# Performance work log

Measured on AMD Instinct MI355X. Metric: run time of the kernel, lower is better.

The kernel has to match this reference:

```python
import jax, jax.numpy as jnp
import numpy as np
from jax.scipy.linalg import solve_triangular

NUM_EMBEDDINGS = 512
EMBEDDING_DIM = 64
SPARSITY = 5
COMMITMENT_COST = 0.25


def batch_omp(data, dictionary, max_nonzero):
    """Batch OMP. data: (M, B), dictionary: (M, N). Returns coeffs (N, B)."""
    M, B = data.shape
    Dt = dictionary.T                       # (N, M)
    G = Dt @ dictionary                     # (N, N) Gram matrix
    h_bar = (Dt @ data).T                   # (B, N)
    h = h_bar
    x = jnp.zeros_like(h_bar)               # (B, N)
    L = jnp.ones((B, 1, 1), data.dtype)     # growing Cholesky factor
    mask = jnp.zeros(h_bar.shape, dtype=bool)
    I = None                                # selected atom indices (B, k)
    bidx = jnp.arange(B)
    for k in range(1, max_nonzero + 1):     # small fixed unroll (5 iters)
        index = jnp.argmax(jnp.abs(h * (~mask)), axis=1)   # (B,)
        mask = mask.at[bidx, index].set(True)
        if k > 1:
            # G[I_b, index_b] for each batch element -> (B, k-1, 1)
            G_stack = G[I, index[:, None]][..., None]
            w = solve_triangular(L, G_stack, lower=True)   # (B, k-1, 1)
            wT = jnp.swapaxes(w, 1, 2)                     # (B, 1, k-1)
            w_corner = jnp.sqrt(jnp.clip(1.0 - jnp.sum(wT ** 2, axis=2, keepdims=True), 0.0))
            top = jnp.concatenate([L, jnp.zeros((B, k - 1, 1), L.dtype)], axis=2)
            bot = jnp.concatenate([wT, w_corner], axis=2)
            L = jnp.concatenate([top, bot], axis=1)        # (B, k, k)
            I = jnp.concatenate([I, index[:, None]], axis=1)
        else:
            I = index[:, None]
        h_stack = jnp.take_along_axis(h_bar, I, axis=1)[..., None]  # (B, k, 1)
        y = solve_triangular(L, h_stack, lower=True)
        x_stack = solve_triangular(jnp.swapaxes(L, 1, 2), y, lower=False)  # (B, k, 1)
        x = x.at[bidx[:, None], I].set(x_stack[..., 0])
        beta = jnp.einsum('bk,bkn->bn', x_stack[..., 0], G[I])  # (B, N)
        h = h_bar - beta
    return x.T                              # (N, B)


def setup_inputs() -> dict:
    key = jax.random.key(0)
    k1, k2 = jax.random.split(key)
    z_e = jax.random.normal(k1, (32, EMBEDDING_DIM, 32, 32), dtype=jnp.float32)
    D = jax.random.normal(k2, (EMBEDDING_DIM, NUM_EMBEDDINGS), dtype=jnp.float32)
    D = D / jnp.linalg.norm(D, axis=0)      # column-normalized atoms (as _normalize_dictionary)
    return {"z_e": z_e, "dictionary": D}


def reference(z_e, dictionary):
    # permute BCHW -> BHWC, then flat view to (embedding_dim, -1) row-major (as torch .view)
    z_perm = jnp.transpose(z_e, (0, 2, 3, 1))          # (B, H, W, C)
    input_shape = z_perm.shape
    ze_flat = z_perm.reshape(EMBEDDING_DIM, -1)        # (M, Btokens)
    coefficients = batch_omp(ze_flat, dictionary, SPARSITY)  # (N, Btokens)
    z_dl = (dictionary @ coefficients).reshape(input_shape)
    e_latent_loss = jnp.mean((jax.lax.stop_gradient(z_dl) - z_perm) ** 2)
    dl_latent_loss = jnp.mean((z_dl - jax.lax.stop_gradient(z_perm)) ** 2)
    loss = COMMITMENT_COST * e_latent_loss + dl_latent_loss
    z_out = z_perm + jax.lax.stop_gradient(z_dl - z_perm)   # straight-through
    return (jnp.transpose(z_out, (0, 3, 1, 2)), loss, coefficients)
```

## Files before the change

### kernel.cpp

```cpp
#include <hip/hip_runtime.h>

#define B_TOTAL 32768
#define NATOM   512
#define MDIM    64
#define KS      5

__global__ void k_perm(const float* __restrict__ ze, float* __restrict__ dT) {
    const int n   = blockIdx.x >> 4;
    const int hw0 = (blockIdx.x & 15) * 64;
    const int t   = threadIdx.x;
    __shared__ float lds[64][65];
#pragma unroll
    for (int r = 0; r < 16; ++r) {
        int id = r * 256 + t;
        int c = id >> 6, i = id & 63;
        lds[c][i] = ze[n * 65536 + c * 1024 + hw0 + i];
    }
    __syncthreads();
#pragma unroll
    for (int r = 0; r < 16; ++r) {
        int id = r * 256 + t;
        int c = id & 63, j = id >> 6;
        int hw = hw0 + j;
        int h = hw >> 5, w = hw & 31;
        int m = (n << 1) | (h >> 4);
        int b = ((h & 15) << 11) | (w << 6) | c;
        dT[m * 32768 + b] = lds[c][j];
    }
}

__global__ void k_gram(const float* __restrict__ D, float* __restrict__ G,
                       float* __restrict__ acc) {
    const int i = blockIdx.x;
    const int t = threadIdx.x;
    __shared__ float col[MDIM];
    if (t < MDIM) col[t] = D[t * NATOM + i];
    __syncthreads();
    for (int j = t; j < NATOM; j += 256) {
        float s = 0.f;
#pragma unroll
        for (int m = 0; m < MDIM; ++m) s = fmaf(col[m], D[m * NATOM + j], s);
        G[i * NATOM + j] = s;
    }
    if (i == 0 && t == 0) *acc = 0.f;
}

__launch_bounds__(256, 2)
__global__ void k_omp(const float* __restrict__ data, const float* __restrict__ D,
                      const float* __restrict__ G, int* __restrict__ idx_out,
                      float* __restrict__ val_out) {
    const int t    = threadIdx.x;
    const int lane = t & 63;
    const int wv   = t >> 6;
    const int b0   = blockIdx.x * 32;

    __shared__ __align__(16) float data_s[32][68];
    __shared__ __align__(16) float stage[4][2048];
    __shared__ int   idx_s[KS][32];
    __shared__ float val_s[KS][32];

#pragma unroll
    for (int r = 0; r < 8; ++r) {
        int id = r * 256 + t;
        int m = id >> 5, bb = id & 31;
        data_s[bb][m] = data[m * B_TOTAL + b0 + bb];
    }
    __syncthreads();

    const float4* __restrict__ D4 = (const float4*)D;
    const float4* __restrict__ G4 = (const float4*)G;

    float4 acc[8][2];
#pragma unroll
    for (int bb = 0; bb < 8; ++bb) {
        acc[bb][0] = make_float4(0.f, 0.f, 0.f, 0.f);
        acc[bb][1] = make_float4(0.f, 0.f, 0.f, 0.f);
    }
    const int bwbase = wv * 8;

#pragma unroll 4
    for (int c = 0; c < 16; ++c) {
        float4 df[4][2];
#pragma unroll
        for (int mm = 0; mm < 4; ++mm) {
            df[mm][0] = D4[(c * 4 + mm) * 128 + lane];
            df[mm][1] = D4[(c * 4 + mm) * 128 + 64 + lane];
        }
#pragma unroll
        for (int bb = 0; bb < 8; ++bb) {
            const float4 dv = *(const float4*)&data_s[bwbase + bb][c * 4];
            const float dm[4] = {dv.x, dv.y, dv.z, dv.w};
#pragma unroll
            for (int mm = 0; mm < 4; ++mm) {
                acc[bb][0].x = fmaf(df[mm][0].x, dm[mm], acc[bb][0].x);
                acc[bb][0].y = fmaf(df[mm][0].y, dm[mm], acc[bb][0].y);
                acc[bb][0].z = fmaf(df[mm][0].z, dm[mm], acc[bb][0].z);
                acc[bb][0].w = fmaf(df[mm][0].w, dm[mm], acc[bb][0].w);
                acc[bb][1].x = fmaf(df[mm][1].x, dm[mm], acc[bb][1].x);
                acc[bb][1].y = fmaf(df[mm][1].y, dm[mm], acc[bb][1].y);
                acc[bb][1].z = fmaf(df[mm][1].z, dm[mm], acc[bb][1].z);
                acc[bb][1].w = fmaf(df[mm][1].w, dm[mm], acc[bb][1].w);
            }
        }
    }

    const int g = lane >> 3;
    const int p = lane & 7;
    float hb[64];
#pragma unroll
    for (int r = 0; r < 2; ++r) {
        __syncthreads();
#pragma unroll
        for (int q2 = 0; q2 < 4; ++q2) {
            int bb = r * 4 + q2;
            *(float4*)&stage[wv][q2 * 512 + 4 * lane]       = acc[bb][0];
            *(float4*)&stage[wv][q2 * 512 + 256 + 4 * lane] = acc[bb][1];
        }
        __syncthreads();
        if ((g >> 2) == r) {
#pragma unroll
            for (int q = 0; q < 16; ++q) {
                const float4 v =
                    *(const float4*)&stage[wv][(g & 3) * 512 + 32 * q + 4 * p];
                hb[4 * q + 0] = v.x;
                hb[4 * q + 1] = v.y;
                hb[4 * q + 2] = v.z;
                hb[4 * q + 3] = v.w;
            }
        }
    }

    float key[64];
#pragma unroll
    for (int e = 0; e < 64; ++e) key[e] = fabsf(hb[e]);

    unsigned msk0 = 0u, msk1 = 0u;
    int   I[KS];
    float xs[KS];
    float gsel[KS];
    float Lm[15];

#pragma unroll
    for (int k = 0; k < KS; ++k) {
        float bv = key[0]; int be = 0; float bhb = hb[0];
#pragma unroll
        for (int e = 1; e < 64; ++e) {
            bool gt = key[e] > bv;
            bv  = gt ? key[e] : bv;
            be  = gt ? e      : be;
            bhb = gt ? hb[e]  : bhb;
        }
        int bn = 32 * (be >> 2) + 4 * p + (be & 3);
#pragma unroll
        for (int off = 1; off < 8; off <<= 1) {
            float ov  = __shfl_xor(bv, off);
            int   on  = __shfl_xor(bn, off);
            float ohb = __shfl_xor(bhb, off);
            bool take = (ov > bv) || (ov == bv && on < bn);
            bv = take ? ov : bv; bn = take ? on : bn; bhb = take ? ohb : bhb;
        }
        const int nsel = bn;
        I[k]    = nsel;
        gsel[k] = bhb;

        {
            int own  = (nsel >> 2) & 7;
            int esel = ((nsel >> 5) << 2) | (nsel & 3);
            if (p == own) {
                if (esel < 32) msk0 |= 1u << esel;
                else           msk1 |= 1u << (esel - 32);
            }
        }

        if (k > 0) {
            float gk[KS - 1], w[KS - 1];
#pragma unroll
            for (int ti = 0; ti < KS - 1; ++ti)
                if (ti < k) gk[ti] = G[I[ti] * NATOM + nsel];
#pragma unroll
            for (int r = 0; r < KS - 1; ++r) {
                if (r < k) {
                    float s = gk[r];
#pragma unroll
                    for (int cc = 0; cc < KS - 1; ++cc)
                        if (cc < r) s -= Lm[r * (r + 1) / 2 + cc] * w[cc];
                    w[r] = s / Lm[r * (r + 1) / 2 + r];
                }
            }
            float s2 = 0.f;
#pragma unroll
            for (int r = 0; r < KS - 1; ++r) if (r < k) s2 += w[r] * w[r];
            float wc = sqrtf(fmaxf(0.f, 1.f - s2));
#pragma unroll
            for (int cc = 0; cc < KS - 1; ++cc)
                if (cc < k) Lm[k * (k + 1) / 2 + cc] = w[cc];
            Lm[k * (k + 1) / 2 + k] = wc;
        } else {
            Lm[0] = 1.f;
        }

        float y[KS];
#pragma unroll
        for (int r = 0; r <= k; ++r) {
            float s = gsel[r];
#pragma unroll
            for (int cc = 0; cc < r; ++cc) s -= Lm[r * (r + 1) / 2 + cc] * y[cc];
            y[r] = s / Lm[r * (r + 1) / 2 + r];
        }
#pragma unroll
        for (int r = k; r >= 0; --r) {
            float s = y[r];
#pragma unroll
            for (int cc = r + 1; cc <= k; ++cc) s -= Lm[cc * (cc + 1) / 2 + r] * xs[cc];
            xs[r] = s / Lm[r * (r + 1) / 2 + r];
        }

        if (k < KS - 1) {
#pragma unroll
            for (int q = 0; q < 16; ++q) {
                float bx = 0.f, by = 0.f, bz = 0.f, bw = 0.f;
#pragma unroll
                for (int ti = 0; ti < KS - 1; ++ti) {
                    if (ti <= k) {
                        const float4 gc = G4[I[ti] * 128 + 8 * q + p];
                        bx = fmaf(xs[ti], gc.x, bx);
                        by = fmaf(xs[ti], gc.y, by);
                        bz = fmaf(xs[ti], gc.z, bz);
                        bw = fmaf(xs[ti], gc.w, bw);
                    }
                }
                {
                    float d0 = hb[4 * q + 0] - bx;
                    float d1 = hb[4 * q + 1] - by;
                    float d2 = hb[4 * q + 2] - bz;
                    float d3 = hb[4 * q + 3] - bw;
                    const int e0 = 4 * q;
                    bool m0 = (e0 + 0 < 32) ? ((msk0 >> (e0 + 0)) & 1u) : ((msk1 >> (e0 - 32)) & 1u);
                    bool m1 = (e0 + 1 < 32) ? ((msk0 >> (e0 + 1)) & 1u) : ((msk1 >> (e0 + 1 - 32)) & 1u);
                    bool m2 = (e0 + 2 < 32) ? ((msk0 >> (e0 + 2)) & 1u) : ((msk1 >> (e0 + 2 - 32)) & 1u);
                    bool m3 = (e0 + 3 < 32) ? ((msk0 >> (e0 + 3)) & 1u) : ((msk1 >> (e0 + 3 - 32)) & 1u);
                    key[e0 + 0] = m0 ? -1.f : fabsf(d0);
                    key[e0 + 1] = m1 ? -1.f : fabsf(d1);
                    key[e0 + 2] = m2 ? -1.f : fabsf(d2);
                    key[e0 + 3] = m3 ? -1.f : fabsf(d3);
                }
            }
        }
    }

    if (p == 0) {
#pragma unroll
        for (int k = 0; k < KS; ++k) {
            idx_s[k][wv * 8 + g] = I[k];
            val_s[k][wv * 8 + g] = xs[k];
        }
    }
    __syncthreads();
    if (t < KS * 32) {
        int k = t >> 5, bb = t & 31;
        idx_out[k * B_TOTAL + b0 + bb] = idx_s[k][bb];
        val_out[k * B_TOTAL + b0 + bb] = val_s[k][bb];
    }
}

__global__ void k_coeff(const int* __restrict__ idx, const float* __restrict__ val,
                        float* __restrict__ coeff) {
    const int bblk = blockIdx.x >> 3;
    const int jc   = blockIdx.x & 7;
    const int b    = bblk * 256 + threadIdx.x;
    int   I[KS]; float V[KS];
#pragma unroll
    for (int k = 0; k < KS; ++k) {
        I[k] = idx[k * B_TOTAL + b];
        V[k] = val[k * B_TOTAL + b];
    }
    const int j0 = jc * 64;
#pragma unroll 4
    for (int j = j0; j < j0 + 64; ++j) {
        float w = 0.f;
#pragma unroll
        for (int k = 0; k < KS; ++k) w = (I[k] == j) ? V[k] : w;
        coeff[j * B_TOTAL + b] = w;
    }
}

__global__ void k_recon(const float* __restrict__ dataT, const float* __restrict__ D,
                        const int* __restrict__ idx, const float* __restrict__ val,
                        float* __restrict__ zout, float* __restrict__ acc) {
    const int n   = blockIdx.x >> 4;
    const int hw0 = (blockIdx.x & 15) * 64;
    const int t   = threadIdx.x;
    __shared__ float lds[64][65];
    float sq = 0.f;
#pragma unroll
    for (int r = 0; r < 16; ++r) {
        int id = r * 256 + t;
        int c = id & 63, j = id >> 6;
        int f = n * 65536 + (hw0 + j) * 64 + c;
        int b = f & 32767;
        int m = f >> 15;
        float zdl = 0.f;
#pragma unroll
        for (int k = 0; k < KS; ++k) {
            int   a = idx[k * B_TOTAL + b];
            float v = val[k * B_TOTAL + b];
            zdl = fmaf(v, D[m * NATOM + a], zdl);
        }
        float zp   = dataT[f];
        float diff = zdl - zp;
        lds[c][j] = zp + diff;
        sq = fmaf(diff, diff, sq);
    }
    __syncthreads();
#pragma unroll
    for (int r = 0; r < 16; ++r) {
        int id = r * 256 + t;
        int cc = id >> 6, i = id & 63;
        zout[n * 65536 + cc * 1024 + hw0 + i] = lds[cc][i];
    }
#pragma unroll
    for (int off = 32; off > 0; off >>= 1) sq += __shfl_xor(sq, off);
    __shared__ float red[4];
    if ((t & 63) == 0) red[t >> 6] = sq;
    __syncthreads();
    if (t == 0) atomicAdd(acc, red[0] + red[1] + red[2] + red[3]);
}

__global__ void k_loss(const float* __restrict__ acc, float* __restrict__ out_loss) {
    if (threadIdx.x == 0 && blockIdx.x == 0)
        *out_loss = 1.25f * (*acc / 2097152.f);
}

extern "C" void kernel_launch(void* const* d_in, const int* in_sizes, int n_in,
                              void* d_out, int out_size, void* d_ws, size_t ws_size,
                              hipStream_t stream) {
    const float* ze = (const float*)d_in[0];
    const float* D  = (const float*)d_in[1];

    float* G     = (float*)d_ws;
    int*   idxp  = (int*)  ((char*)d_ws + (size_t)262144 * 4);
    float* valp  = (float*)((char*)d_ws + (size_t)(262144 + 163840) * 4);
    float* accp  = (float*)((char*)d_ws + (size_t)(262144 + 2 * 163840) * 4);
    float* dataT = (float*)((char*)d_ws + (size_t)(262144 + 2 * 163840 + 64) * 4);

    float* zout  = (float*)d_out;
    float* lossp = zout + 2097152;
    float* coeff = zout + 2097153;

    k_perm <<<512, 256, 0, stream>>>(ze, dataT);
    k_gram <<<512, 256, 0, stream>>>(D, G, accp);
    k_omp  <<<1024, 256, 0, stream>>>(dataT, D, G, idxp, valp);
    k_coeff<<<1024, 256, 0, stream>>>(idxp, valp, coeff);
    k_recon<<<512, 256, 0, stream>>>(dataT, D, idxp, valp, zout, accp);
    k_loss <<<1, 64, 0, stream>>>(accp, lossp);
}
```

Baseline: 185.8 us.

## Merge prep kernels, raise OMP occupancy, tree argmax, reciprocal divides, vectorize coeff

Fuses the permute and Gram kernels into one launch split by block index, which saves a kernel launch. In the OMP kernel it overlays the data and staging shared buffers in a single array and raises launch bounds from 2 to 3 blocks per CU. It also replaces the serial 64-element argmax with chunked partial maxima plus a tree reduction, and replaces the triangular-solve divisions with cached reciprocals of the diagonal. The coefficient scatter kernel now handles four tokens per thread with int4/float4 loads and stores. The tighter register budget could cause spills of the 64-entry per-thread arrays. The float4 stores go to an output pointer offset by one float, so they are unaligned.

```diff
diff --git a/kernel.cpp b/kernel.cpp
--- a/kernel.cpp
+++ b/kernel.cpp
@@ -5,47 +5,47 @@
 #define MDIM    64
 #define KS      5
 
-__global__ void k_perm(const float* __restrict__ ze, float* __restrict__ dT) {
-    const int n   = blockIdx.x >> 4;
-    const int hw0 = (blockIdx.x & 15) * 64;
-    const int t   = threadIdx.x;
-    __shared__ float lds[64][65];
-#pragma unroll
-    for (int r = 0; r < 16; ++r) {
-        int id = r * 256 + t;
-        int c = id >> 6, i = id & 63;
-        lds[c][i] = ze[n * 65536 + c * 1024 + hw0 + i];
-    }
-    __syncthreads();
-#pragma unroll
-    for (int r = 0; r < 16; ++r) {
-        int id = r * 256 + t;
-        int c = id & 63, j = id >> 6;
-        int hw = hw0 + j;
-        int h = hw >> 5, w = hw & 31;
-        int m = (n << 1) | (h >> 4);
-        int b = ((h & 15) << 11) | (w << 6) | c;
-        dT[m * 32768 + b] = lds[c][j];
-    }
-}
-
-__global__ void k_gram(const float* __restrict__ D, float* __restrict__ G,
+__global__ void k_prep(const float* __restrict__ ze, float* __restrict__ dT,
+                       const float* __restrict__ D, float* __restrict__ G,
                        float* __restrict__ acc) {
-    const int i = blockIdx.x;
     const int t = threadIdx.x;
-    __shared__ float col[MDIM];
-    if (t < MDIM) col[t] = D[t * NATOM + i];
-    __syncthreads();
-    for (int j = t; j < NATOM; j += 256) {
-        float s = 0.f;
-#pragma unroll
-        for (int m = 0; m < MDIM; ++m) s = fmaf(col[m], D[m * NATOM + j], s);
-        G[i * NATOM + j] = s;
-    }
-    if (i == 0 && t == 0) *acc = 0.f;
-}
-
-__launch_bounds__(256, 2)
+    if (blockIdx.x < 512) {
+        const int n   = blockIdx.x >> 4;
+        const int hw0 = (blockIdx.x & 15) * 64;
+        __shared__ float lds[64][65];
+#pragma unroll
+        for (int r = 0; r < 16; ++r) {
+            int id = r * 256 + t;
+            int c = id >> 6, i = id & 63;
+            lds[c][i] = ze[n * 65536 + c * 1024 + hw0 + i];
+        }
+        __syncthreads();
+#pragma unroll
+        for (int r = 0; r < 16; ++r) {
+            int id = r * 256 + t;
+            int c = id & 63, j = id >> 6;
+            int hw = hw0 + j;
+            int h = hw >> 5, w = hw & 31;
+            int m = (n << 1) | (h >> 4);
+            int b = ((h & 15) << 11) | (w << 6) | c;
+            dT[m * 32768 + b] = lds[c][j];
+        }
+    } else {
+        const int i = blockIdx.x - 512;
+        __shared__ float col[MDIM];
+        if (t < MDIM) col[t] = D[t * NATOM + i];
+        __syncthreads();
+        for (int j = t; j < NATOM; j += 256) {
+            float s = 0.f;
+#pragma unroll
+            for (int m = 0; m < MDIM; ++m) s = fmaf(col[m], D[m * NATOM + j], s);
+            G[i * NATOM + j] = s;
+        }
+        if (i == 0 && t == 0) *acc = 0.f;
+    }
+}
+
+__launch_bounds__(256, 3)
 __global__ void k_omp(const float* __restrict__ data, const float* __restrict__ D,
                       const float* __restrict__ G, int* __restrict__ idx_out,
                       float* __restrict__ val_out) {
@@ -54,16 +54,16 @@
     const int wv   = t >> 6;
     const int b0   = blockIdx.x * 32;
 
-    __shared__ __align__(16) float data_s[32][68];
-    __shared__ __align__(16) float stage[4][2048];
+    __shared__ __align__(16) float uni[8192];
     __shared__ int   idx_s[KS][32];
     __shared__ float val_s[KS][32];
+#define DATA_S(bb, m) uni[(bb) * 68 + (m)]
 
 #pragma unroll
     for (int r = 0; r < 8; ++r) {
         int id = r * 256 + t;
         int m = id >> 5, bb = id & 31;
-        data_s[bb][m] = data[m * B_TOTAL + b0 + bb];
+        DATA_S(bb, m) = data[m * B_TOTAL + b0 + bb];
     }
     __syncthreads();
 
@@ -88,7 +88,7 @@
         }
 #pragma unroll
         for (int bb = 0; bb < 8; ++bb) {
-            const float4 dv = *(const float4*)&data_s[bwbase + bb][c * 4];
+            const float4 dv = *(const float4*)&DATA_S(bwbase + bb, c * 4);
             const float dm[4] = {dv.x, dv.y, dv.z, dv.w};
 #pragma unroll
             for (int mm = 0; mm < 4; ++mm) {
@@ -113,15 +113,15 @@
 #pragma unroll
         for (int q2 = 0; q2 < 4; ++q2) {
             int bb = r * 4 + q2;
-            *(float4*)&stage[wv][q2 * 512 + 4 * lane]       = acc[bb][0];
-            *(float4*)&stage[wv][q2 * 512 + 256 + 4 * lane] = acc[bb][1];
+            *(float4*)&uni[wv * 2048 + q2 * 512 + 4 * lane]       = acc[bb][0];
+            *(float4*)&uni[wv * 2048 + q2 * 512 + 256 + 4 * lane] = acc[bb][1];
         }
         __syncthreads();
         if ((g >> 2) == r) {
 #pragma unroll
             for (int q = 0; q < 16; ++q) {
                 const float4 v =
-                    *(const float4*)&stage[wv][(g & 3) * 512 + 32 * q + 4 * p];
+                    *(const float4*)&uni[wv * 2048 + (g & 3) * 512 + 32 * q + 4 * p];
                 hb[4 * q + 0] = v.x;
                 hb[4 * q + 1] = v.y;
                 hb[4 * q + 2] = v.z;
@@ -139,18 +139,37 @@
     float xs[KS];
     float gsel[KS];
     float Lm[15];
+    float invD[KS];
 
 #pragma unroll
     for (int k = 0; k < KS; ++k) {
-        float bv = key[0]; int be = 0; float bhb = hb[0];
-#pragma unroll
-        for (int e = 1; e < 64; ++e) {
-            bool gt = key[e] > bv;
-            bv  = gt ? key[e] : bv;
-            be  = gt ? e      : be;
-            bhb = gt ? hb[e]  : bhb;
-        }
-        int bn = 32 * (be >> 2) + 4 * p + (be & 3);
+        float cv[8]; int ce[8]; float ch[8];
+#pragma unroll
+        for (int c0 = 0; c0 < 8; ++c0) {
+            float bv0 = key[8 * c0]; int be0 = 8 * c0; float bh0 = hb[8 * c0];
+#pragma unroll
+            for (int e = 1; e < 8; ++e) {
+                int ee = 8 * c0 + e;
+                bool gt = key[ee] > bv0;
+                bv0 = gt ? key[ee] : bv0;
+                be0 = gt ? ee      : be0;
+                bh0 = gt ? hb[ee]  : bh0;
+            }
+            cv[c0] = bv0; ce[c0] = be0; ch[c0] = bh0;
+        }
+#pragma unroll
+        for (int s = 1; s < 8; s <<= 1) {
+#pragma unroll
+            for (int c0 = 0; c0 < 8; c0 += 2 * s) {
+                bool gt = cv[c0 + s] > cv[c0];
+                cv[c0] = gt ? cv[c0 + s] : cv[c0];
+                ce[c0] = gt ? ce[c0 + s] : ce[c0];
+                ch[c0] = gt ? ch[c0 + s] : ch[c0];
+            }
+        }
+        float bv = cv[0]; float bhb = ch[0];
+        int   bn = 32 * (ce[0] >> 2) + 4 * p + (ce[0] & 3);
+
 #pragma unroll
         for (int off = 1; off < 8; off <<= 1) {
             float ov  = __shfl_xor(bv, off);
@@ -184,7 +203,7 @@
 #pragma unroll
                     for (int cc = 0; cc < KS - 1; ++cc)
                         if (cc < r) s -= Lm[r * (r + 1) / 2 + cc] * w[cc];
-                    w[r] = s / Lm[r * (r + 1) / 2 + r];
+                    w[r] = s * invD[r];
                 }
             }
             float s2 = 0.f;
@@ -195,8 +214,10 @@
             for (int cc = 0; cc < KS - 1; ++cc)
                 if (cc < k) Lm[k * (k + 1) / 2 + cc] = w[cc];
             Lm[k * (k + 1) / 2 + k] = wc;
+            invD[k] = 1.0f / wc;
         } else {
             Lm[0] = 1.f;
+            invD[0] = 1.f;
         }
 
         float y[KS];
@@ -205,14 +226,14 @@
             float s = gsel[r];
 #pragma unroll
             for (int cc = 0; cc < r; ++cc) s -= Lm[r * (r + 1) / 2 + cc] * y[cc];
-            y[r] = s / Lm[r * (r + 1) / 2 + r];
+            y[r] = s * invD[r];
         }
 #pragma unroll
         for (int r = k; r >= 0; --r) {
             float s = y[r];
 #pragma unroll
             for (int cc = r + 1; cc <= k; ++cc) s -= Lm[cc * (cc + 1) / 2 + r] * xs[cc];
-            xs[r] = s / Lm[r * (r + 1) / 2 + r];
+            xs[r] = s * invD[r];
         }
 
         if (k < KS - 1) {
@@ -261,26 +282,32 @@
         idx_out[k * B_TOTAL + b0 + bb] = idx_s[k][bb];
         val_out[k * B_TOTAL + b0 + bb] = val_s[k][bb];
     }
+#undef DATA_S
 }
 
 __global__ void k_coeff(const int* __restrict__ idx, const float* __restrict__ val,
                         float* __restrict__ coeff) {
-    const int bblk = blockIdx.x >> 3;
+    const int tile = blockIdx.x >> 3;
     const int jc   = blockIdx.x & 7;
-    const int b    = bblk * 256 + threadIdx.x;
-    int   I[KS]; float V[KS];
+    const int b4   = tile * 1024 + threadIdx.x * 4;
+    int4   I[KS]; float4 V[KS];
 #pragma unroll
     for (int k = 0; k < KS; ++k) {
-        I[k] = idx[k * B_TOTAL + b];
-        V[k] = val[k * B_TOTAL + b];
+        I[k] = *(const int4*)  &idx[k * B_TOTAL + b4];
+        V[k] = *(const float4*)&val[k * B_TOTAL + b4];
     }
     const int j0 = jc * 64;
 #pragma unroll 4
     for (int j = j0; j < j0 + 64; ++j) {
-        float w = 0.f;
-#pragma unroll
-        for (int k = 0; k < KS; ++k) w = (I[k] == j) ? V[k] : w;
-        coeff[j * B_TOTAL + b] = w;
+        float4 w = make_float4(0.f, 0.f, 0.f, 0.f);
+#pragma unroll
+        for (int k = 0; k < KS; ++k) {
+            w.x = (I[k].x == j) ? V[k].x : w.x;
+            w.y = (I[k].y == j) ? V[k].y : w.y;
+            w.z = (I[k].z == j) ? V[k].z : w.z;
+            w.w = (I[k].w == j) ? V[k].w : w.w;
+        }
+        *(float4*)&coeff[j * B_TOTAL + b4] = w;
     }
 }
 
@@ -347,10 +374,9 @@
     float* lossp = zout + 2097152;
     float* coeff = zout + 2097153;
 
-    k_perm <<<512, 256, 0, stream>>>(ze, dataT);
-    k_gram <<<512, 256, 0, stream>>>(D, G, accp);
+    k_prep <<<1024, 256, 0, stream>>>(ze, dataT, D, G, accp);
     k_omp  <<<1024, 256, 0, stream>>>(dataT, D, G, idxp, valp);
-    k_coeff<<<1024, 256, 0, stream>>>(idxp, valp, coeff);
+    k_coeff<<<256, 256, 0, stream>>>(idxp, valp, coeff);
     k_recon<<<512, 256, 0, stream>>>(dataT, D, idxp, valp, zout, accp);
     k_loss <<<1, 64, 0, stream>>>(accp, lossp);
 }
```

Result: slower. 352.5 us (+89.6%).
